# Kernel tuning notes

Hardware: AMD Instinct MI355X
Metric: run time of the kernel (lower is better)

The kernel has to match this reference:

```python
import jax, jax.numpy as jnp
import numpy as np

B, L, D, H = 2, 4096, 512, 8
HD = D // H
SCALE = 1.0 / (D / H) ** 0.5


def setup_inputs() -> dict:
    key = jax.random.key(0)
    ks = jax.random.split(key, 12)
    s = 0.02
    inp = {
        "q": jax.random.normal(ks[0], (B, L, D), jnp.float32),
        "k": jax.random.normal(ks[1], (B, L, D), jnp.float32),
        "v": jax.random.normal(ks[2], (B, L, D), jnp.float32),
        # causal mask, True = keep (masked_fill where mask == False)
        "mask": jnp.tril(jnp.ones((L, L), bool))[None, None, :, :],
        "Wq": jax.random.normal(ks[3], (D, D), jnp.float32) * s,
        "bq": jnp.zeros((D,), jnp.float32),
        "Wk": jax.random.normal(ks[4], (D, D), jnp.float32) * s,
        "bk": jnp.zeros((D,), jnp.float32),
        "Wv": jax.random.normal(ks[5], (D, D), jnp.float32) * s,
        "bv": jnp.zeros((D,), jnp.float32),
        "Wo": jax.random.normal(ks[6], (D, D), jnp.float32) * s,
        "bo": jnp.zeros((D,), jnp.float32),
    }
    return inp


def _split_heads(x):
    # [B, L, D] -> [B, H, L, HD]
    b, l, d = x.shape
    return x.reshape(b, l, H, HD).transpose(0, 2, 1, 3)


def reference(q, k, v, mask, Wq, bq, Wk, bk, Wv, bv, Wo, bo):
    # Dropout is inference-mode (identity), matching module.eval().
    qh = _split_heads(q @ Wq.T + bq)          # [B,H,L,HD]
    kh = _split_heads(k @ Wk.T + bk)          # [B,H,L,HD]
    vh = _split_heads(v @ Wv.T + bv)          # [B,H,L,HD]
    scores = jnp.einsum("bhqd,bhkd->bhqk", qh, kh) * SCALE
    scores = jnp.where(mask, scores, -jnp.inf)
    attn = jax.nn.softmax(scores, axis=-1)
    out = jnp.einsum("bhqk,bhkd->bhqd", attn, vh)  # [B,H,L,HD]
    out = out.transpose(0, 2, 1, 3).reshape(q.shape[0], q.shape[1], D)
    return out @ Wo.T + bo
```

## Files before the change

### kernel.cpp

```cpp
#include <hip/hip_runtime.h>

typedef __bf16 bf16;
typedef __bf16 bf16x4 __attribute__((ext_vector_type(4)));
typedef __bf16 bf16x8 __attribute__((ext_vector_type(8)));
typedef float  f32x4  __attribute__((ext_vector_type(4)));
typedef float  f32x16 __attribute__((ext_vector_type(16)));
typedef unsigned int u32x2 __attribute__((ext_vector_type(2)));
typedef unsigned int u32x4 __attribute__((ext_vector_type(4)));

#define NB   2
#define NL   4096
#define ND   512
#define NH   8
#define NHD  64

static __device__ __forceinline__ void g2l16(const bf16* g, bf16* l) {
    __builtin_amdgcn_global_load_lds(
        (const __attribute__((address_space(1))) unsigned int*)g,
        (__attribute__((address_space(3))) unsigned int*)l, 16, 0, 0);
}

__global__ __launch_bounds__(256, 2) void proj_qkv(
    const float* __restrict__ q, const float* __restrict__ k, const float* __restrict__ v,
    const float* __restrict__ Wq, const float* __restrict__ Wk, const float* __restrict__ Wv,
    const float* __restrict__ biasq, const float* __restrict__ biask, const float* __restrict__ biasv,
    bf16* __restrict__ qh, bf16* __restrict__ kh, bf16* __restrict__ vt)
{
    const int z = blockIdx.z;
    const float* X    = (z == 0) ? q : (z == 1) ? k : v;
    const float* W    = (z == 0) ? Wq : (z == 1) ? Wk : Wv;
    const float* bias = (z == 0) ? biasq : (z == 1) ? biask : biasv;

    const int m0 = blockIdx.y * 128;
    const int n0 = blockIdx.x * 128;

    __shared__ bf16 smem[32768];

    const int t    = threadIdx.x;
    const int lane = t & 63;
    const int wm   = (t >> 7) & 1;
    const int wn   = (t >> 6) & 1;
    const int quad = lane >> 4;
    const int l16  = lane & 15;

    f32x4 ta[8], tb[8];
    auto issue = [&](int k0) {
        #pragma unroll
        for (int p = 0; p < 8; ++p) {
            const int c4 = p * 256 + t;
            const int r = c4 >> 4, cs = c4 & 15;
            ta[p] = *(const f32x4*)(X + (size_t)(m0 + r) * ND + k0 + cs * 4);
            tb[p] = *(const f32x4*)(W + (size_t)(n0 + r) * ND + k0 + cs * 4);
        }
    };
    auto commit = [&](int buf) {
        bf16* Ad = smem + buf * 8192;
        bf16* Bd = smem + 16384 + buf * 8192;
        #pragma unroll
        for (int p = 0; p < 8; ++p) {
            const int c4 = p * 256 + t;
            const int r = c4 >> 4, cs = c4 & 15;
            const int addr = r * 64 + (((cs >> 1) ^ (r & 7)) * 8) + (cs & 1) * 4;
            bf16x4 a4, b4;
            #pragma unroll
            for (int j = 0; j < 4; ++j) { a4[j] = (bf16)ta[p][j]; b4[j] = (bf16)tb[p][j]; }
            *(bf16x4*)(Ad + addr) = a4;
            *(bf16x4*)(Bd + addr) = b4;
        }
    };

    f32x4 acc[4][4] = {};
    issue(0);

    for (int it = 0; it < 8; ++it) {
        commit(it & 1);
        __syncthreads();
        if (it + 1 < 8) issue((it + 1) * 64);

        const bf16* as = smem + (it & 1) * 8192;
        const bf16* bs = smem + 16384 + (it & 1) * 8192;
        #pragma unroll
        for (int kk = 0; kk < 2; ++kk) {
            bf16x8 aF[4], bF[4];
            #pragma unroll
            for (int i = 0; i < 4; ++i) {
                const int ra = wm * 64 + i * 16 + l16;
                const int rb = wn * 64 + i * 16 + l16;
                aF[i] = *(const bf16x8*)(as + ra * 64 + (((kk * 4 + quad) ^ (ra & 7)) * 8));
                bF[i] = *(const bf16x8*)(bs + rb * 64 + (((kk * 4 + quad) ^ (rb & 7)) * 8));
            }
            #pragma unroll
            for (int mt = 0; mt < 4; ++mt)
                #pragma unroll
                for (int nt = 0; nt < 4; ++nt)
                    acc[mt][nt] = __builtin_amdgcn_mfma_f32_16x16x32_bf16(
                        aF[mt], bF[nt], acc[mt][nt], 0, 0, 0);
        }
    }

    __syncthreads();
    const float oscale = (z == 0) ? 0.125f : (z == 1) ? 1.4426950408889634f : 1.0f;
    const int b = m0 >> 12;
    const int l0 = m0 & 4095;
    bf16* Cs = smem;

    if (z == 2) {
        #pragma unroll
        for (int nt = 0; nt < 4; ++nt) {
            const int col = wn * 64 + nt * 16 + l16;
            const float bb = bias[n0 + col];
            #pragma unroll
            for (int mt = 0; mt < 4; ++mt) {
                const int rowm = wm * 64 + mt * 16 + quad * 4;
                #pragma unroll
                for (int rb = 0; rb < 4; ++rb)
                    Cs[col * 136 + rowm + rb] = (bf16)(acc[mt][nt][rb] + bb);
            }
        }
        __syncthreads();
        #pragma unroll
        for (int p = 0; p < 8; ++p) {
            const int id = p * 256 + t;
            const int c = id >> 4, kc = id & 15;
            const int gcol = n0 + c;
            const int h = gcol >> 6, hd = gcol & 63;
            const bf16x8 v8 = *(const bf16x8*)(Cs + c * 136 + kc * 8);
            *(bf16x8*)(vt + ((size_t)(b * NH + h) * NHD + hd) * NL + l0 + kc * 8) = v8;
        }
    } else {
        #pragma unroll
        for (int nt = 0; nt < 4; ++nt) {
            const int col = wn * 64 + nt * 16 + l16;
            const float bb = bias[n0 + col];
            #pragma unroll
            for (int mt = 0; mt < 4; ++mt) {
                const int rowm = wm * 64 + mt * 16 + quad * 4;
                #pragma unroll
                for (int rb = 0; rb < 4; ++rb)
                    Cs[(rowm + rb) * 136 + col] = (bf16)((acc[mt][nt][rb] + bb) * oscale);
            }
        }
        __syncthreads();
        bf16* dst = (z == 0) ? qh : kh;
        const int h0 = n0 >> 6;
        #pragma unroll
        for (int p = 0; p < 8; ++p) {
            const int id = p * 256 + t;
            const int r = id >> 4, j = (id >> 3) & 1, kc = id & 7;
            const bf16x8 v8 = *(const bf16x8*)(Cs + r * 136 + j * 64 + kc * 8);
            *(bf16x8*)(dst + ((size_t)(b * NH + h0 + j) * NL + l0 + r) * NHD + kc * 8) = v8;
        }
    }
}

__global__ __launch_bounds__(512, 2) void attn(
    const bf16* __restrict__ qh, const bf16* __restrict__ kh,
    const bf16* __restrict__ vt, bf16* __restrict__ ao)
{
    const int bh  = blockIdx.x;
    const int b   = bh >> 3, h = bh & 7;
    const int qtA = blockIdx.y;
    const int qtB = 31 - qtA;
    const int nAp = qtA + 1;

    __shared__ bf16 smem[65536];

    const int t    = threadIdx.x;
    const int wave = t >> 6;
    const int g    = wave >> 2;
    const int w4   = wave & 3;
    const int lane = t & 63;
    const int l32  = lane & 31;
    const int half = lane >> 5;
    const int sb   = g * 32768;
    const int tg   = t & 255;

    const bf16* Qg = qh + (size_t)bh * NL * NHD;
    const bf16* Kg = kh + (size_t)bh * NL * NHD;
    const bf16* Vg = vt + (size_t)bh * NHD * NL;

    #pragma unroll
    for (int p = 0; p < 4; ++p) {
        const int id = p * 512 + t;
        const int tile = id >> 10, r = (id >> 3) & 127, s = id & 7;
        const int q0 = (tile ? qtB : qtA) * 128;
        g2l16(Qg + (size_t)(q0 + r) * NHD + s * 8, smem + id * 8);
    }
    __syncthreads();

    bf16x8 qf[4];
    {
        const int qoff = (g == 0) ? 8192 : 0;
        #pragma unroll
        for (int c = 0; c < 4; ++c)
            qf[c] = *(const bf16x8*)(smem + qoff + (w4 * 32 + l32) * 64 + c * 16 + half * 8);
    }
    __syncthreads();

    auto stage_kv = [&](int k0, int buf) {
        bf16* kd = smem + sb + buf * 16384;
        bf16* vd = kd + 8192;
        #pragma unroll
        for (int p = 0; p < 4; ++p) {
            const int id = p * 256 + tg;
            const int r = id >> 3, s = id & 7;
            g2l16(Kg + (size_t)(k0 + r) * NHD + ((s ^ (r & 7)) * 8), kd + id * 8);
            const int ks2 = id >> 9, idh = id & 511;
            const int r2 = idh >> 3, s2 = idh & 7;
            g2l16(Vg + (size_t)r2 * NL + k0 + ks2 * 64 + ((s2 ^ (r2 & 7)) * 8),
                  vd + id * 8);
        }
    };

    stage_kv(((g == 0) ? (15 - qtA) : 0) * 128, 0);

    f32x16 o_acc[2] = {};
    float l_lane = 0.f;

    for (int jj = 0; jj < 17; ++jj) {
        __syncthreads();

        if (jj + 1 < 17) {
            const int jn = jj + 1;
            if (g == 0)          stage_kv((15 - qtA + jn) * 128, jn & 1);
            else if (jn < 16)    stage_kv(((jn < nAp) ? jn : jn - nAp) * 128, jn & 1);
        }

        if (g == 1 && jj == nAp) {
            const float lt = l_lane + __shfl_xor(l_lane, 32, 64);
            const float rcp = 1.0f / fmaxf(lt, 1e-20f);
            const int row = qtA * 128 + w4 * 32 + l32;
            #pragma unroll
            for (int mt2 = 0; mt2 < 2; ++mt2)
                #pragma unroll
                for (int rr = 0; rr < 4; ++rr) {
                    const int hd = mt2 * 32 + rr * 8 + half * 4;
                    bf16x4 val;
                    #pragma unroll
                    for (int rb = 0; rb < 4; ++rb)
                        val[rb] = (bf16)(o_acc[mt2][rr * 4 + rb] * rcp);
                    *(bf16x4*)(ao + ((size_t)b * NL + row) * ND + h * NHD + hd) = val;
                }
            o_acc[0] = (f32x16)(0.f); o_acc[1] = (f32x16)(0.f);
            l_lane = 0.f;
            const bf16* Qt = Qg + (size_t)(qtB * 128 + w4 * 32 + l32) * NHD;
            #pragma unroll
            for (int c = 0; c < 4; ++c)
                qf[c] = *(const bf16x8*)(Qt + c * 16 + half * 8);
        }

        const bool act = (g == 0) || (jj < 16);
        if (act) {
            const bool onA   = (g == 1) && (jj < nAp);
            const int tile   = (g == 0) ? (15 - qtA + jj) : (onA ? jj : jj - nAp);
            const int qt_cur = onA ? qtA : qtB;
            const bf16* kb_ = smem + sb + (jj & 1) * 16384;
            const bf16* vb_ = kb_ + 8192;
            const int qrow_l = w4 * 32 + l32;

            #pragma unroll
            for (int ksub = 0; ksub < 2; ++ksub) {
                const bf16* ks_ = kb_ + ksub * 4096;
                const bf16* vs_ = vb_ + ksub * 4096;
                const int j64 = tile * 2 + ksub;

                f32x16 sacc[2] = {};
                #pragma unroll
                for (int c = 0; c < 4; ++c) {
                    #pragma unroll
                    for (int mt = 0; mt < 2; ++mt) {
                        const int row   = mt * 32 + l32;
                        const int chunk = 2 * c + half;
                        const bf16x8 kf = *(const bf16x8*)(ks_ + row * 64 + ((chunk ^ (row & 7)) * 8));
                        sacc[mt] = __builtin_amdgcn_mfma_f32_32x32x16_bf16(
                            kf, qf[c], sacc[mt], 0, 0, 0);
                    }
                }

                const bool diag = (j64 >= 2 * qt_cur);
                const int  dq   = j64 * 64 - qt_cur * 128;
                #pragma unroll
                for (int mt = 0; mt < 2; ++mt) {
                    #pragma unroll
                    for (int r = 0; r < 16; ++r) {
                        const int kv = mt * 32 + (r & 3) + 8 * (r >> 2) + 4 * half;
                        float e;
                        if (diag && (dq + kv > qrow_l)) e = 0.f;
                        else e = __builtin_amdgcn_exp2f(sacc[mt][r]);
                        l_lane += e;
                        sacc[mt][r] = e;
                    }
                }

                #pragma unroll
                for (int c = 0; c < 4; ++c) {
                    const int mt = c >> 1;
                    const int b0 = (c & 1) * 8;
                    unsigned w0, w1, w2, w3;
                    asm("v_cvt_pk_bf16_f32 %0, %1, %2" : "=v"(w0)
                        : "v"(sacc[mt][b0 + 0]), "v"(sacc[mt][b0 + 1]));
                    asm("v_cvt_pk_bf16_f32 %0, %1, %2" : "=v"(w1)
                        : "v"(sacc[mt][b0 + 2]), "v"(sacc[mt][b0 + 3]));
                    asm("v_cvt_pk_bf16_f32 %0, %1, %2" : "=v"(w2)
                        : "v"(sacc[mt][b0 + 4]), "v"(sacc[mt][b0 + 5]));
                    asm("v_cvt_pk_bf16_f32 %0, %1, %2" : "=v"(w3)
                        : "v"(sacc[mt][b0 + 6]), "v"(sacc[mt][b0 + 7]));
                    const u32x2 s02 = __builtin_amdgcn_permlane32_swap(w0, w2, false, false);
                    const u32x2 s13 = __builtin_amdgcn_permlane32_swap(w1, w3, false, false);
                    u32x4 pw_ = { s02.x, s13.x, s02.y, s13.y };
                    bf16x8 pf;
                    __builtin_memcpy(&pf, &pw_, 16);
                    #pragma unroll
                    for (int mt2 = 0; mt2 < 2; ++mt2) {
                        const int row = mt2 * 32 + l32;
                        const int u8  = 2 * c + half;
                        const bf16x8 vf = *(const bf16x8*)(vs_ + row * 64 + ((u8 ^ (row & 7)) * 8));
                        o_acc[mt2] = __builtin_amdgcn_mfma_f32_32x32x16_bf16(
                            vf, pf, o_acc[mt2], 0, 0, 0);
                    }
                }
            }
        }
    }

    __syncthreads();
    float* comb = (float*)smem;
    if (g == 1) {
        const int base = w4 * (64 * 36) + lane * 36;
        #pragma unroll
        for (int mt2 = 0; mt2 < 2; ++mt2)
            #pragma unroll
            for (int i = 0; i < 16; ++i)
                comb[base + mt2 * 16 + i] = o_acc[mt2][i];
        const float lt = l_lane + __shfl_xor(l_lane, 32, 64);
        if (half == 0) comb[9216 + w4 * 32 + l32] = lt;
    }
    __syncthreads();
    if (g == 0) {
        const int base = w4 * (64 * 36) + lane * 36;
        const float lt = l_lane + __shfl_xor(l_lane, 32, 64)
                       + comb[9216 + w4 * 32 + l32];
        const float rcp = 1.0f / fmaxf(lt, 1e-20f);
        const int row = qtB * 128 + w4 * 32 + l32;
        #pragma unroll
        for (int mt2 = 0; mt2 < 2; ++mt2)
            #pragma unroll
            for (int rr = 0; rr < 4; ++rr) {
                const int hd = mt2 * 32 + rr * 8 + half * 4;
                bf16x4 val;
                #pragma unroll
                for (int rb = 0; rb < 4; ++rb)
                    val[rb] = (bf16)((o_acc[mt2][rr * 4 + rb] +
                                      comb[base + mt2 * 16 + rr * 4 + rb]) * rcp);
                *(bf16x4*)(ao + ((size_t)b * NL + row) * ND + h * NHD + hd) = val;
            }
    }
}

__global__ __launch_bounds__(256, 2) void out_proj(
    const bf16* __restrict__ ao, const float* __restrict__ wo,
    const float* __restrict__ bo, float* __restrict__ out)
{
    const int m0 = blockIdx.y * 128;
    const int n0 = blockIdx.x * 128;

    __shared__ bf16 smem[34816];

    const int t    = threadIdx.x;
    const int lane = t & 63;
    const int wm   = (t >> 7) & 1;
    const int wn   = (t >> 6) & 1;
    const int quad = lane >> 4;
    const int l16  = lane & 15;

    bf16x8 va[4];
    f32x4  tb[8];
    auto issue = [&](int k0) {
        #pragma unroll
        for (int p = 0; p < 4; ++p) {
            const int c8 = p * 256 + t;
            const int r = c8 >> 3, s = c8 & 7;
            va[p] = *(const bf16x8*)(ao + (size_t)(m0 + r) * ND + k0 + s * 8);
        }
        #pragma unroll
        for (int p = 0; p < 8; ++p) {
            const int c4 = p * 256 + t;
            const int r = c4 >> 4, cs = c4 & 15;
            tb[p] = *(const f32x4*)(wo + (size_t)(n0 + r) * ND + k0 + cs * 4);
        }
    };
    auto commit = [&](int buf) {
        bf16* Ad = smem + buf * 8192;
        bf16* Bd = smem + 16384 + buf * 8192;
        #pragma unroll
        for (int p = 0; p < 4; ++p) {
            const int c8 = p * 256 + t;
            const int r = c8 >> 3, s = c8 & 7;
            *(bf16x8*)(Ad + r * 64 + ((s ^ (r & 7)) * 8)) = va[p];
        }
        #pragma unroll
        for (int p = 0; p < 8; ++p) {
            const int c4 = p * 256 + t;
            const int r = c4 >> 4, cs = c4 & 15;
            const int addr = r * 64 + (((cs >> 1) ^ (r & 7)) * 8) + (cs & 1) * 4;
            bf16x4 b4;
            #pragma unroll
            for (int j = 0; j < 4; ++j) b4[j] = (bf16)tb[p][j];
            *(bf16x4*)(Bd + addr) = b4;
        }
    };

    f32x4 acc[4][4] = {};
    issue(0);

    for (int it = 0; it < 8; ++it) {
        commit(it & 1);
        __syncthreads();
        if (it + 1 < 8) issue((it + 1) * 64);

        const bf16* as = smem + (it & 1) * 8192;
        const bf16* bs = smem + 16384 + (it & 1) * 8192;
        #pragma unroll
        for (int kk = 0; kk < 2; ++kk) {
            bf16x8 aF[4], bF[4];
            #pragma unroll
            for (int i = 0; i < 4; ++i) {
                const int ra = wm * 64 + i * 16 + l16;
                const int rb = wn * 64 + i * 16 + l16;
                aF[i] = *(const bf16x8*)(as + ra * 64 + (((kk * 4 + quad) ^ (ra & 7)) * 8));
                bF[i] = *(const bf16x8*)(bs + rb * 64 + (((kk * 4 + quad) ^ (rb & 7)) * 8));
            }
            #pragma unroll
            for (int mt = 0; mt < 4; ++mt)
                #pragma unroll
                for (int nt = 0; nt < 4; ++nt)
                    acc[mt][nt] = __builtin_amdgcn_mfma_f32_16x16x32_bf16(
                        aF[mt], bF[nt], acc[mt][nt], 0, 0, 0);
        }
    }

    __syncthreads();
    float* Cs = (float*)smem;
    #pragma unroll
    for (int nt = 0; nt < 4; ++nt) {
        const int col = wn * 64 + nt * 16 + l16;
        const float bb = bo[n0 + col];
        #pragma unroll
        for (int mt = 0; mt < 4; ++mt) {
            const int rowm = wm * 64 + mt * 16 + quad * 4;
            #pragma unroll
            for (int rb = 0; rb < 4; ++rb)
                Cs[(rowm + rb) * 132 + col] = acc[mt][nt][rb] + bb;
        }
    }
    __syncthreads();
    #pragma unroll
    for (int p = 0; p < 16; ++p) {
        const int id = p * 256 + t;
        const int r = id >> 5, kc = id & 31;
        const f32x4 v4 = *(const f32x4*)(Cs + r * 132 + kc * 4);
        *(f32x4*)(out + (size_t)(m0 + r) * ND + n0 + kc * 4) = v4;
    }
}

extern "C" void kernel_launch(void* const* d_in, const int* in_sizes, int n_in,
                              void* d_out, int out_size, void* d_ws, size_t ws_size,
                              hipStream_t stream) {
    (void)in_sizes; (void)n_in; (void)out_size; (void)ws_size;

    const float* q  = (const float*)d_in[0];
    const float* k  = (const float*)d_in[1];
    const float* v  = (const float*)d_in[2];
    const float* Wq = (const float*)d_in[4];
    const float* bq = (const float*)d_in[5];
    const float* Wk = (const float*)d_in[6];
    const float* bk = (const float*)d_in[7];
    const float* Wv = (const float*)d_in[8];
    const float* bv = (const float*)d_in[9];
    const float* Wo = (const float*)d_in[10];
    const float* bo = (const float*)d_in[11];

    const size_t XSZ = (size_t)NB * NL * ND;
    bf16* p = (bf16*)d_ws;
    bf16* qh  = p; p += XSZ;
    bf16* kh  = p; p += XSZ;
    bf16* vt  = p; p += XSZ;
    bf16* ao  = p; p += XSZ;

    dim3 g1(ND / 128, (NB * NL) / 128, 3);
    proj_qkv<<<g1, 256, 0, stream>>>(q, k, v, Wq, Wk, Wv, bq, bk, bv, qh, kh, vt);

    dim3 g2(16, 16, 1);
    attn<<<g2, 512, 0, stream>>>(qh, kh, vt, ao);

    dim3 g3(ND / 128, (NB * NL) / 128, 1);
    out_proj<<<g3, 256, 0, stream>>>(ao, Wo, bo, (float*)d_out);
}
```

Measured before the change: 248.7 us.

## Fuse QKV projection, attention and output projection into one persistent kernel

Result: slower. 309.3 us (+24.4%).

```diff
diff --git a/kernel.cpp b/kernel.cpp
--- a/kernel.cpp
+++ b/kernel.cpp
@@ -20,446 +20,459 @@
         (__attribute__((address_space(3))) unsigned int*)l, 16, 0, 0);
 }
 
-__global__ __launch_bounds__(256, 2) void proj_qkv(
+__device__ __forceinline__ void gbar(unsigned* c) {
+    __syncthreads();
+    if (threadIdx.x == 0) {
+        __threadfence();
+        atomicAdd(c, 1u);
+        while (atomicAdd(c, 0u) < 256u) __builtin_amdgcn_s_sleep(8);
+        __threadfence();
+    }
+    __syncthreads();
+}
+
+__global__ __launch_bounds__(512, 2) void fused(
     const float* __restrict__ q, const float* __restrict__ k, const float* __restrict__ v,
     const float* __restrict__ Wq, const float* __restrict__ Wk, const float* __restrict__ Wv,
-    const float* __restrict__ biasq, const float* __restrict__ biask, const float* __restrict__ biasv,
-    bf16* __restrict__ qh, bf16* __restrict__ kh, bf16* __restrict__ vt)
+    const float* __restrict__ bq, const float* __restrict__ bk, const float* __restrict__ bv,
+    const float* __restrict__ Wo, const float* __restrict__ bo,
+    bf16* __restrict__ qh, bf16* __restrict__ kh, bf16* __restrict__ vt,
+    bf16* __restrict__ ao, float* __restrict__ out, unsigned* __restrict__ ctr)
 {
-    const int z = blockIdx.z;
-    const float* X    = (z == 0) ? q : (z == 1) ? k : v;
-    const float* W    = (z == 0) ? Wq : (z == 1) ? Wk : Wv;
-    const float* bias = (z == 0) ? biasq : (z == 1) ? biask : biasv;
-
-    const int m0 = blockIdx.y * 128;
-    const int n0 = blockIdx.x * 128;
-
-    __shared__ bf16 smem[32768];
-
+    __shared__ bf16 smem[65536];
+
+    const int bid  = blockIdx.x;
     const int t    = threadIdx.x;
     const int lane = t & 63;
-    const int wm   = (t >> 7) & 1;
-    const int wn   = (t >> 6) & 1;
-    const int quad = lane >> 4;
-    const int l16  = lane & 15;
-
-    f32x4 ta[8], tb[8];
-    auto issue = [&](int k0) {
+
+    {
+        const int wave = t >> 6;
+        const int wm   = wave >> 2;
+        const int wn   = wave & 3;
+        const int quad = lane >> 4;
+        const int l16  = lane & 15;
+        const int m0 = (bid >> 2) * 128;
+        const int n0 = (bid & 3) * 128;
+        const int b  = m0 >> 12;
+        const int l0 = m0 & 4095;
+
+        for (int zi = 0; zi < 3; ++zi) {
+            const float* X    = (zi == 0) ? q  : (zi == 1) ? k  : v;
+            const float* W    = (zi == 0) ? Wq : (zi == 1) ? Wk : Wv;
+            const float* bias = (zi == 0) ? bq : (zi == 1) ? bk : bv;
+
+            f32x4 ta[8], tb[8];
+            auto issue = [&](int k0) {
+                #pragma unroll
+                for (int p = 0; p < 8; ++p) {
+                    const int c4 = p * 512 + t;
+                    const int r = c4 >> 5, cs = c4 & 31;
+                    ta[p] = *(const f32x4*)(X + (size_t)(m0 + r) * ND + k0 + cs * 4);
+                    tb[p] = *(const f32x4*)(W + (size_t)(n0 + r) * ND + k0 + cs * 4);
+                }
+            };
+            auto commit = [&](int buf) {
+                bf16* Ad = smem + buf * 16384;
+                bf16* Bd = smem + 32768 + buf * 16384;
+                #pragma unroll
+                for (int p = 0; p < 8; ++p) {
+                    const int c4 = p * 512 + t;
+                    const int r = c4 >> 5, cs = c4 & 31;
+                    const int addr = r * 128 + ((((cs >> 1) ^ (r & 7))) * 8) + (cs & 1) * 4;
+                    bf16x4 a4, b4;
+                    #pragma unroll
+                    for (int j = 0; j < 4; ++j) { a4[j] = (bf16)ta[p][j]; b4[j] = (bf16)tb[p][j]; }
+                    *(bf16x4*)(Ad + addr) = a4;
+                    *(bf16x4*)(Bd + addr) = b4;
+                }
+            };
+
+            f32x4 acc[4][2] = {};
+            issue(0);
+            for (int it = 0; it < 4; ++it) {
+                commit(it & 1);
+                __syncthreads();
+                if (it + 1 < 4) issue((it + 1) * 128);
+
+                const bf16* as = smem + (it & 1) * 16384;
+                const bf16* bs = smem + 32768 + (it & 1) * 16384;
+                #pragma unroll
+                for (int kk = 0; kk < 4; ++kk) {
+                    bf16x8 aF[4], bF[2];
+                    #pragma unroll
+                    for (int i = 0; i < 4; ++i) {
+                        const int ra = wm * 64 + i * 16 + l16;
+                        aF[i] = *(const bf16x8*)(as + ra * 128 + (((kk * 4 + quad) ^ (ra & 7)) * 8));
+                    }
+                    #pragma unroll
+                    for (int j = 0; j < 2; ++j) {
+                        const int rb = wn * 32 + j * 16 + l16;
+                        bF[j] = *(const bf16x8*)(bs + rb * 128 + (((kk * 4 + quad) ^ (rb & 7)) * 8));
+                    }
+                    #pragma unroll
+                    for (int mt = 0; mt < 4; ++mt)
+                        #pragma unroll
+                        for (int nt = 0; nt < 2; ++nt)
+                            acc[mt][nt] = __builtin_amdgcn_mfma_f32_16x16x32_bf16(
+                                aF[mt], bF[nt], acc[mt][nt], 0, 0, 0);
+                }
+            }
+
+            __syncthreads();
+            const float oscale = (zi == 0) ? 0.125f : (zi == 1) ? 1.4426950408889634f : 1.0f;
+            bf16* Cs = smem;
+
+            if (zi == 2) {
+                #pragma unroll
+                for (int nt = 0; nt < 2; ++nt) {
+                    const int col = wn * 32 + nt * 16 + l16;
+                    const float bb = bias[n0 + col];
+                    #pragma unroll
+                    for (int mt = 0; mt < 4; ++mt) {
+                        const int rowm = wm * 64 + mt * 16 + quad * 4;
+                        #pragma unroll
+                        for (int rb = 0; rb < 4; ++rb)
+                            Cs[col * 136 + rowm + rb] = (bf16)(acc[mt][nt][rb] + bb);
+                    }
+                }
+                __syncthreads();
+                #pragma unroll
+                for (int p = 0; p < 4; ++p) {
+                    const int id = p * 512 + t;
+                    const int c = id >> 4, kc = id & 15;
+                    const int gcol = n0 + c;
+                    const int h = gcol >> 6, hd = gcol & 63;
+                    const bf16x8 v8 = *(const bf16x8*)(Cs + c * 136 + kc * 8);
+                    *(bf16x8*)(vt + ((size_t)(b * NH + h) * NHD + hd) * NL + l0 + kc * 8) = v8;
+                }
+            } else {
+                #pragma unroll
+                for (int nt = 0; nt < 2; ++nt) {
+                    const int col = wn * 32 + nt * 16 + l16;
+                    const float bb = bias[n0 + col];
+                    #pragma unroll
+                    for (int mt = 0; mt < 4; ++mt) {
+                        const int rowm = wm * 64 + mt * 16 + quad * 4;
+                        #pragma unroll
+                        for (int rb = 0; rb < 4; ++rb)
+                            Cs[(rowm + rb) * 136 + col] = (bf16)((acc[mt][nt][rb] + bb) * oscale);
+                    }
+                }
+                __syncthreads();
+                bf16* dst = (zi == 0) ? qh : kh;
+                const int h0 = n0 >> 6;
+                #pragma unroll
+                for (int p = 0; p < 4; ++p) {
+                    const int id = p * 512 + t;
+                    const int r = id >> 4, j = (id >> 3) & 1, kc = id & 7;
+                    const bf16x8 v8 = *(const bf16x8*)(Cs + r * 136 + j * 64 + kc * 8);
+                    *(bf16x8*)(dst + ((size_t)(b * NH + h0 + j) * NL + l0 + r) * NHD + kc * 8) = v8;
+                }
+            }
+            __syncthreads();
+        }
+    }
+
+    gbar(ctr);
+
+    {
+        const int bh  = bid >> 4;
+        const int b   = bh >> 3, h = bh & 7;
+        const int qtA = bid & 15;
+        const int qtB = 31 - qtA;
+        const int nAp = qtA + 1;
+
+        const int wave = t >> 6;
+        const int g    = wave >> 2;
+        const int w4   = wave & 3;
+        const int l32  = lane & 31;
+        const int half = lane >> 5;
+        const int sb   = g * 32768;
+        const int tg   = t & 255;
+
+        const bf16* Qg = qh + (size_t)bh * NL * NHD;
+        const bf16* Kg = kh + (size_t)bh * NL * NHD;
+        const bf16* Vg = vt + (size_t)bh * NHD * NL;
+
         #pragma unroll
-        for (int p = 0; p < 8; ++p) {
-            const int c4 = p * 256 + t;
-            const int r = c4 >> 4, cs = c4 & 15;
-            ta[p] = *(const f32x4*)(X + (size_t)(m0 + r) * ND + k0 + cs * 4);
-            tb[p] = *(const f32x4*)(W + (size_t)(n0 + r) * ND + k0 + cs * 4);
-        }
-    };
-    auto commit = [&](int buf) {
-        bf16* Ad = smem + buf * 8192;
-        bf16* Bd = smem + 16384 + buf * 8192;
+        for (int p = 0; p < 4; ++p) {
+            const int id = p * 512 + t;
+            const int tile = id >> 10, r = (id >> 3) & 127, s = id & 7;
+            const int q0 = (tile ? qtB : qtA) * 128;
+            g2l16(Qg + (size_t)(q0 + r) * NHD + s * 8, smem + id * 8);
+        }
+        __syncthreads();
+
+        bf16x8 qf[4];
+        {
+            const int qoff = (g == 0) ? 8192 : 0;
+            #pragma unroll
+            for (int c = 0; c < 4; ++c)
+                qf[c] = *(const bf16x8*)(smem + qoff + (w4 * 32 + l32) * 64 + c * 16 + half * 8);
+        }
+        __syncthreads();
+
+        auto stage_kv = [&](int k0, int buf) {
+            bf16* kd = smem + sb + buf * 16384;
+            bf16* vd = kd + 8192;
+            #pragma unroll
+            for (int p = 0; p < 4; ++p) {
+                const int id = p * 256 + tg;
+                const int r = id >> 3, s = id & 7;
+                g2l16(Kg + (size_t)(k0 + r) * NHD + ((s ^ (r & 7)) * 8), kd + id * 8);
+                const int ks2 = id >> 9, idh = id & 511;
+                const int r2 = idh >> 3, s2 = idh & 7;
+                g2l16(Vg + (size_t)r2 * NL + k0 + ks2 * 64 + ((s2 ^ (r2 & 7)) * 8),
+                      vd + id * 8);
+            }
+        };
+
+        stage_kv(((g == 0) ? (15 - qtA) : 0) * 128, 0);
+
+        f32x16 o_acc[2] = {};
+        float l_lane = 0.f;
+
+        for (int jj = 0; jj < 17; ++jj) {
+            __syncthreads();
+
+            if (jj + 1 < 17) {
+                const int jn = jj + 1;
+                if (g == 0)          stage_kv((15 - qtA + jn) * 128, jn & 1);
+                else if (jn < 16)    stage_kv(((jn < nAp) ? jn : jn - nAp) * 128, jn & 1);
+            }
+
+            if (g == 1 && jj == nAp) {
+                const float lt = l_lane + __shfl_xor(l_lane, 32, 64);
+                const float rcp = 1.0f / fmaxf(lt, 1e-20f);
+                const int row = qtA * 128 + w4 * 32 + l32;
+                #pragma unroll
+                for (int mt2 = 0; mt2 < 2; ++mt2)
+                    #pragma unroll
+                    for (int rr = 0; rr < 4; ++rr) {
+                        const int hd = mt2 * 32 + rr * 8 + half * 4;
+                        bf16x4 val;
+                        #pragma unroll
+                        for (int rb = 0; rb < 4; ++rb)
+                            val[rb] = (bf16)(o_acc[mt2][rr * 4 + rb] * rcp);
+                        *(bf16x4*)(ao + ((size_t)b * NL + row) * ND + h * NHD + hd) = val;
+                    }
+                o_acc[0] = (f32x16)(0.f); o_acc[1] = (f32x16)(0.f);
+                l_lane = 0.f;
+                const bf16* Qt = Qg + (size_t)(qtB * 128 + w4 * 32 + l32) * NHD;
+                #pragma unroll
+                for (int c = 0; c < 4; ++c)
+                    qf[c] = *(const bf16x8*)(Qt + c * 16 + half * 8);
+            }
+
+            const bool act = (g == 0) || (jj < 16);
+            if (act) {
+                const bool onA   = (g == 1) && (jj < nAp);
+                const int tile   = (g == 0) ? (15 - qtA + jj) : (onA ? jj : jj - nAp);
+                const int qt_cur = onA ? qtA : qtB;
+                const bf16* kb_ = smem + sb + (jj & 1) * 16384;
+                const bf16* vb_ = kb_ + 8192;
+                const int qrow_l = w4 * 32 + l32;
+
+                #pragma unroll
+                for (int ksub = 0; ksub < 2; ++ksub) {
+                    const bf16* ks_ = kb_ + ksub * 4096;
+                    const bf16* vs_ = vb_ + ksub * 4096;
+                    const int j64 = tile * 2 + ksub;
+
+                    f32x16 sacc[2] = {};
+                    #pragma unroll
+                    for (int c = 0; c < 4; ++c) {
+                        #pragma unroll
+                        for (int mt = 0; mt < 2; ++mt) {
+                            const int row   = mt * 32 + l32;
+                            const int chunk = 2 * c + half;
+                            const bf16x8 kf = *(const bf16x8*)(ks_ + row * 64 + ((chunk ^ (row & 7)) * 8));
+                            sacc[mt] = __builtin_amdgcn_mfma_f32_32x32x16_bf16(
+                                kf, qf[c], sacc[mt], 0, 0, 0);
+                        }
+                    }
+
+                    const bool diag = (j64 >= 2 * qt_cur);
+                    const int  dq   = j64 * 64 - qt_cur * 128;
+                    #pragma unroll
+                    for (int mt = 0; mt < 2; ++mt) {
+                        #pragma unroll
+                        for (int r = 0; r < 16; ++r) {
+                            const int kv = mt * 32 + (r & 3) + 8 * (r >> 2) + 4 * half;
+                            float e;
+                            if (diag && (dq + kv > qrow_l)) e = 0.f;
+                            else e = __builtin_amdgcn_exp2f(sacc[mt][r]);
+                            l_lane += e;
+                            sacc[mt][r] = e;
+                        }
+                    }
+
+                    #pragma unroll
+                    for (int c = 0; c < 4; ++c) {
+                        const int mt = c >> 1;
+                        const int b0 = (c & 1) * 8;
+                        unsigned w0, w1, w2, w3;
+                        asm("v_cvt_pk_bf16_f32 %0, %1, %2" : "=v"(w0)
+                            : "v"(sacc[mt][b0 + 0]), "v"(sacc[mt][b0 + 1]));
+                        asm("v_cvt_pk_bf16_f32 %0, %1, %2" : "=v"(w1)
+                            : "v"(sacc[mt][b0 + 2]), "v"(sacc[mt][b0 + 3]));
+                        asm("v_cvt_pk_bf16_f32 %0, %1, %2" : "=v"(w2)
+                            : "v"(sacc[mt][b0 + 4]), "v"(sacc[mt][b0 + 5]));
+                        asm("v_cvt_pk_bf16_f32 %0, %1, %2" : "=v"(w3)
+                            : "v"(sacc[mt][b0 + 6]), "v"(sacc[mt][b0 + 7]));
+                        const u32x2 s02 = __builtin_amdgcn_permlane32_swap(w0, w2, false, false);
+                        const u32x2 s13 = __builtin_amdgcn_permlane32_swap(w1, w3, false, false);
+                        u32x4 pw_ = { s02.x, s13.x, s02.y, s13.y };
+                        bf16x8 pf;
+                        __builtin_memcpy(&pf, &pw_, 16);
+                        #pragma unroll
+                        for (int mt2 = 0; mt2 < 2; ++mt2) {
+                            const int row = mt2 * 32 + l32;
+                            const int u8  = 2 * c + half;
+                            const bf16x8 vf = *(const bf16x8*)(vs_ + row * 64 + ((u8 ^ (row & 7)) * 8));
+                            o_acc[mt2] = __builtin_amdgcn_mfma_f32_32x32x16_bf16(
+                                vf, pf, o_acc[mt2], 0, 0, 0);
+                        }
+                    }
+                }
+            }
+        }
+
+        __syncthreads();
+        float* comb = (float*)smem;
+        if (g == 1) {
+            const int base = w4 * (64 * 36) + lane * 36;
+            #pragma unroll
+            for (int mt2 = 0; mt2 < 2; ++mt2)
+                #pragma unroll
+                for (int i = 0; i < 16; ++i)
+                    comb[base + mt2 * 16 + i] = o_acc[mt2][i];
+            const float lt = l_lane + __shfl_xor(l_lane, 32, 64);
+            if (half == 0) comb[9216 + w4 * 32 + l32] = lt;
+        }
+        __syncthreads();
+        if (g == 0) {
+            const int base = w4 * (64 * 36) + lane * 36;
+            const float lt = l_lane + __shfl_xor(l_lane, 32, 64)
+                           + comb[9216 + w4 * 32 + l32];
+            const float rcp = 1.0f / fmaxf(lt, 1e-20f);
+            const int row = qtB * 128 + w4 * 32 + l32;
+            #pragma unroll
+            for (int mt2 = 0; mt2 < 2; ++mt2)
+                #pragma unroll
+                for (int rr = 0; rr < 4; ++rr) {
+                    const int hd = mt2 * 32 + rr * 8 + half * 4;
+                    bf16x4 val;
+                    #pragma unroll
+                    for (int rb = 0; rb < 4; ++rb)
+                        val[rb] = (bf16)((o_acc[mt2][rr * 4 + rb] +
+                                          comb[base + mt2 * 16 + rr * 4 + rb]) * rcp);
+                    *(bf16x4*)(ao + ((size_t)b * NL + row) * ND + h * NHD + hd) = val;
+                }
+        }
+    }
+
+    gbar(ctr + 1);
+
+    {
+        const int wave = t >> 6;
+        const int wm   = wave >> 2;
+        const int wn   = wave & 3;
+        const int quad = lane >> 4;
+        const int l16  = lane & 15;
+        const int m0 = (bid >> 2) * 128;
+        const int n0 = (bid & 3) * 128;
+
+        bf16x8 va[4];
+        f32x4  tb[8];
+        auto issue = [&](int k0) {
+            #pragma unroll
+            for (int p = 0; p < 4; ++p) {
+                const int c8 = p * 512 + t;
+                const int r = c8 >> 4, s = c8 & 15;
+                va[p] = *(const bf16x8*)(ao + (size_t)(m0 + r) * ND + k0 + s * 8);
+            }
+            #pragma unroll
+            for (int p = 0; p < 8; ++p) {
+                const int c4 = p * 512 + t;
+                const int r = c4 >> 5, cs = c4 & 31;
+                tb[p] = *(const f32x4*)(Wo + (size_t)(n0 + r) * ND + k0 + cs * 4);
+            }
+        };
+        auto commit = [&](int buf) {
+            bf16* Ad = smem + buf * 16384;
+            bf16* Bd = smem + 32768 + buf * 16384;
+            #pragma unroll
+            for (int p = 0; p < 4; ++p) {
+                const int c8 = p * 512 + t;
+                const int r = c8 >> 4, s = c8 & 15;
+                *(bf16x8*)(Ad + r * 128 + ((s ^ (r & 7)) * 8)) = va[p];
+            }
+            #pragma unroll
+            for (int p = 0; p < 8; ++p) {
+                const int c4 = p * 512 + t;
+                const int r = c4 >> 5, cs = c4 & 31;
+                const int addr = r * 128 + ((((cs >> 1) ^ (r & 7))) * 8) + (cs & 1) * 4;
+                bf16x4 b4;
+                #pragma unroll
+                for (int j = 0; j < 4; ++j) b4[j] = (bf16)tb[p][j];
+                *(bf16x4*)(Bd + addr) = b4;
+            }
+        };
+
+        f32x4 acc[4][2] = {};
+        issue(0);
+        for (int it = 0; it < 4; ++it) {
+            commit(it & 1);
+            __syncthreads();
+            if (it + 1 < 4) issue((it + 1) * 128);
+
+            const bf16* as = smem + (it & 1) * 16384;
+            const bf16* bs = smem + 32768 + (it & 1) * 16384;
+            #pragma unroll
+            for (int kk = 0; kk < 4; ++kk) {
+                bf16x8 aF[4], bF[2];
+                #pragma unroll
+                for (int i = 0; i < 4; ++i) {
+                    const int ra = wm * 64 + i * 16 + l16;
+                    aF[i] = *(const bf16x8*)(as + ra * 128 + (((kk * 4 + quad) ^ (ra & 7)) * 8));
+                }
+                #pragma unroll
+                for (int j = 0; j < 2; ++j) {
+                    const int rb = wn * 32 + j * 16 + l16;
+                    bF[j] = *(const bf16x8*)(bs + rb * 128 + (((kk * 4 + quad) ^ (rb & 7)) * 8));
+                }
+                #pragma unroll
+                for (int mt = 0; mt < 4; ++mt)
+                    #pragma unroll
+                    for (int nt = 0; nt < 2; ++nt)
+                        acc[mt][nt] = __builtin_amdgcn_mfma_f32_16x16x32_bf16(
+                            aF[mt], bF[nt], acc[mt][nt], 0, 0, 0);
+            }
+        }
+
+        __syncthreads();
+        float* Cs = (float*)smem;
         #pragma unroll
-        for (int p = 0; p < 8; ++p) {
-            const int c4 = p * 256 + t;
-            const int r = c4 >> 4, cs = c4 & 15;
-            const int addr = r * 64 + (((cs >> 1) ^ (r & 7)) * 8) + (cs & 1) * 4;
-            bf16x4 a4, b4;
-            #pragma unroll
-            for (int j = 0; j < 4; ++j) { a4[j] = (bf16)ta[p][j]; b4[j] = (bf16)tb[p][j]; }
-            *(bf16x4*)(Ad + addr) = a4;
-            *(bf16x4*)(Bd + addr) = b4;
-        }
-    };
-
-    f32x4 acc[4][4] = {};
-    issue(0);
-
-    for (int it = 0; it < 8; ++it) {
-        commit(it & 1);
-        __syncthreads();
-        if (it + 1 < 8) issue((it + 1) * 64);
-
-        const bf16* as = smem + (it & 1) * 8192;
-        const bf16* bs = smem + 16384 + (it & 1) * 8192;
-        #pragma unroll
-        for (int kk = 0; kk < 2; ++kk) {
-            bf16x8 aF[4], bF[4];
-            #pragma unroll
-            for (int i = 0; i < 4; ++i) {
-                const int ra = wm * 64 + i * 16 + l16;
-                const int rb = wn * 64 + i * 16 + l16;
-                aF[i] = *(const bf16x8*)(as + ra * 64 + (((kk * 4 + quad) ^ (ra & 7)) * 8));
-                bF[i] = *(const bf16x8*)(bs + rb * 64 + (((kk * 4 + quad) ^ (rb & 7)) * 8));
-            }
-            #pragma unroll
-            for (int mt = 0; mt < 4; ++mt)
-                #pragma unroll
-                for (int nt = 0; nt < 4; ++nt)
-                    acc[mt][nt] = __builtin_amdgcn_mfma_f32_16x16x32_bf16(
-                        aF[mt], bF[nt], acc[mt][nt], 0, 0, 0);
-        }
-    }
-
-    __syncthreads();
-    const float oscale = (z == 0) ? 0.125f : (z == 1) ? 1.4426950408889634f : 1.0f;
-    const int b = m0 >> 12;
-    const int l0 = m0 & 4095;
-    bf16* Cs = smem;
-
-    if (z == 2) {
-        #pragma unroll
-        for (int nt = 0; nt < 4; ++nt) {
-            const int col = wn * 64 + nt * 16 + l16;
-            const float bb = bias[n0 + col];
+        for (int nt = 0; nt < 2; ++nt) {
+            const int col = wn * 32 + nt * 16 + l16;
+            const float bb = bo[n0 + col];
             #pragma unroll
             for (int mt = 0; mt < 4; ++mt) {
                 const int rowm = wm * 64 + mt * 16 + quad * 4;
                 #pragma unroll
                 for (int rb = 0; rb < 4; ++rb)
-                    Cs[col * 136 + rowm + rb] = (bf16)(acc[mt][nt][rb] + bb);
+                    Cs[(rowm + rb) * 132 + col] = acc[mt][nt][rb] + bb;
             }
         }
         __syncthreads();
         #pragma unroll
         for (int p = 0; p < 8; ++p) {
-            const int id = p * 256 + t;
-            const int c = id >> 4, kc = id & 15;
-            const int gcol = n0 + c;
-            const int h = gcol >> 6, hd = gcol & 63;
-            const bf16x8 v8 = *(const bf16x8*)(Cs + c * 136 + kc * 8);
-            *(bf16x8*)(vt + ((size_t)(b * NH + h) * NHD + hd) * NL + l0 + kc * 8) = v8;
-        }
-    } else {
-        #pragma unroll
-        for (int nt = 0; nt < 4; ++nt) {
-            const int col = wn * 64 + nt * 16 + l16;
-            const float bb = bias[n0 + col];
-            #pragma unroll
-            for (int mt = 0; mt < 4; ++mt) {
-                const int rowm = wm * 64 + mt * 16 + quad * 4;
-                #pragma unroll
-                for (int rb = 0; rb < 4; ++rb)
-                    Cs[(rowm + rb) * 136 + col] = (bf16)((acc[mt][nt][rb] + bb) * oscale);
-            }
-        }
-        __syncthreads();
-        bf16* dst = (z == 0) ? qh : kh;
-        const int h0 = n0 >> 6;
-        #pragma unroll
-        for (int p = 0; p < 8; ++p) {
-            const int id = p * 256 + t;
-            const int r = id >> 4, j = (id >> 3) & 1, kc = id & 7;
-            const bf16x8 v8 = *(const bf16x8*)(Cs + r * 136 + j * 64 + kc * 8);
-            *(bf16x8*)(dst + ((size_t)(b * NH + h0 + j) * NL + l0 + r) * NHD + kc * 8) = v8;
-        }
-    }
-}
-
-__global__ __launch_bounds__(512, 2) void attn(
-    const bf16* __restrict__ qh, const bf16* __restrict__ kh,
-    const bf16* __restrict__ vt, bf16* __restrict__ ao)
-{
-    const int bh  = blockIdx.x;
-    const int b   = bh >> 3, h = bh & 7;
-    const int qtA = blockIdx.y;
-    const int qtB = 31 - qtA;
-    const int nAp = qtA + 1;
-
-    __shared__ bf16 smem[65536];
-
-    const int t    = threadIdx.x;
-    const int wave = t >> 6;
-    const int g    = wave >> 2;
-    const int w4   = wave & 3;
-    const int lane = t & 63;
-    const int l32  = lane & 31;
-    const int half = lane >> 5;
-    const int sb   = g * 32768;
-    const int tg   = t & 255;
-
-    const bf16* Qg = qh + (size_t)bh * NL * NHD;
-    const bf16* Kg = kh + (size_t)bh * NL * NHD;
-    const bf16* Vg = vt + (size_t)bh * NHD * NL;
-
-    #pragma unroll
-    for (int p = 0; p < 4; ++p) {
-        const int id = p * 512 + t;
-        const int tile = id >> 10, r = (id >> 3) & 127, s = id & 7;
-        const int q0 = (tile ? qtB : qtA) * 128;
-        g2l16(Qg + (size_t)(q0 + r) * NHD + s * 8, smem + id * 8);
-    }
-    __syncthreads();
-
-    bf16x8 qf[4];
-    {
-        const int qoff = (g == 0) ? 8192 : 0;
-        #pragma unroll
-        for (int c = 0; c < 4; ++c)
-            qf[c] = *(const bf16x8*)(smem + qoff + (w4 * 32 + l32) * 64 + c * 16 + half * 8);
-    }
-    __syncthreads();
-
-    auto stage_kv = [&](int k0, int buf) {
-        bf16* kd = smem + sb + buf * 16384;
-        bf16* vd = kd + 8192;
-        #pragma unroll
-        for (int p = 0; p < 4; ++p) {
-            const int id = p * 256 + tg;
-            const int r = id >> 3, s = id & 7;
-            g2l16(Kg + (size_t)(k0 + r) * NHD + ((s ^ (r & 7)) * 8), kd + id * 8);
-            const int ks2 = id >> 9, idh = id & 511;
-            const int r2 = idh >> 3, s2 = idh & 7;
-            g2l16(Vg + (size_t)r2 * NL + k0 + ks2 * 64 + ((s2 ^ (r2 & 7)) * 8),
-                  vd + id * 8);
-        }
-    };
-
-    stage_kv(((g == 0) ? (15 - qtA) : 0) * 128, 0);
-
-    f32x16 o_acc[2] = {};
-    float l_lane = 0.f;
-
-    for (int jj = 0; jj < 17; ++jj) {
-        __syncthreads();
-
-        if (jj + 1 < 17) {
-            const int jn = jj + 1;
-            if (g == 0)          stage_kv((15 - qtA + jn) * 128, jn & 1);
-            else if (jn < 16)    stage_kv(((jn < nAp) ? jn : jn - nAp) * 128, jn & 1);
-        }
-
-        if (g == 1 && jj == nAp) {
-            const float lt = l_lane + __shfl_xor(l_lane, 32, 64);
-            const float rcp = 1.0f / fmaxf(lt, 1e-20f);
-            const int row = qtA * 128 + w4 * 32 + l32;
-            #pragma unroll
-            for (int mt2 = 0; mt2 < 2; ++mt2)
-                #pragma unroll
-                for (int rr = 0; rr < 4; ++rr) {
-                    const int hd = mt2 * 32 + rr * 8 + half * 4;
-                    bf16x4 val;
-                    #pragma unroll
-                    for (int rb = 0; rb < 4; ++rb)
-                        val[rb] = (bf16)(o_acc[mt2][rr * 4 + rb] * rcp);
-                    *(bf16x4*)(ao + ((size_t)b * NL + row) * ND + h * NHD + hd) = val;
-                }
-            o_acc[0] = (f32x16)(0.f); o_acc[1] = (f32x16)(0.f);
-            l_lane = 0.f;
-            const bf16* Qt = Qg + (size_t)(qtB * 128 + w4 * 32 + l32) * NHD;
-            #pragma unroll
-            for (int c = 0; c < 4; ++c)
-                qf[c] = *(const bf16x8*)(Qt + c * 16 + half * 8);
-        }
-
-        const bool act = (g == 0) || (jj < 16);
-        if (act) {
-            const bool onA   = (g == 1) && (jj < nAp);
-            const int tile   = (g == 0) ? (15 - qtA + jj) : (onA ? jj : jj - nAp);
-            const int qt_cur = onA ? qtA : qtB;
-            const bf16* kb_ = smem + sb + (jj & 1) * 16384;
-            const bf16* vb_ = kb_ + 8192;
-            const int qrow_l = w4 * 32 + l32;
-
-            #pragma unroll
-            for (int ksub = 0; ksub < 2; ++ksub) {
-                const bf16* ks_ = kb_ + ksub * 4096;
-                const bf16* vs_ = vb_ + ksub * 4096;
-                const int j64 = tile * 2 + ksub;
-
-                f32x16 sacc[2] = {};
-                #pragma unroll
-                for (int c = 0; c < 4; ++c) {
-                    #pragma unroll
-                    for (int mt = 0; mt < 2; ++mt) {
-                        const int row   = mt * 32 + l32;
-                        const int chunk = 2 * c + half;
-                        const bf16x8 kf = *(const bf16x8*)(ks_ + row * 64 + ((chunk ^ (row & 7)) * 8));
-                        sacc[mt] = __builtin_amdgcn_mfma_f32_32x32x16_bf16(
-                            kf, qf[c], sacc[mt], 0, 0, 0);
-                    }
-                }
-
-                const bool diag = (j64 >= 2 * qt_cur);
-                const int  dq   = j64 * 64 - qt_cur * 128;
-                #pragma unroll
-                for (int mt = 0; mt < 2; ++mt) {
-                    #pragma unroll
-                    for (int r = 0; r < 16; ++r) {
-                        const int kv = mt * 32 + (r & 3) + 8 * (r >> 2) + 4 * half;
-                        float e;
-                        if (diag && (dq + kv > qrow_l)) e = 0.f;
-                        else e = __builtin_amdgcn_exp2f(sacc[mt][r]);
-                        l_lane += e;
-                        sacc[mt][r] = e;
-                    }
-                }
-
-                #pragma unroll
-                for (int c = 0; c < 4; ++c) {
-                    const int mt = c >> 1;
-                    const int b0 = (c & 1) * 8;
-                    unsigned w0, w1, w2, w3;
-                    asm("v_cvt_pk_bf16_f32 %0, %1, %2" : "=v"(w0)
-                        : "v"(sacc[mt][b0 + 0]), "v"(sacc[mt][b0 + 1]));
-                    asm("v_cvt_pk_bf16_f32 %0, %1, %2" : "=v"(w1)
-                        : "v"(sacc[mt][b0 + 2]), "v"(sacc[mt][b0 + 3]));
-                    asm("v_cvt_pk_bf16_f32 %0, %1, %2" : "=v"(w2)
-                        : "v"(sacc[mt][b0 + 4]), "v"(sacc[mt][b0 + 5]));
-                    asm("v_cvt_pk_bf16_f32 %0, %1, %2" : "=v"(w3)
-                        : "v"(sacc[mt][b0 + 6]), "v"(sacc[mt][b0 + 7]));
-                    const u32x2 s02 = __builtin_amdgcn_permlane32_swap(w0, w2, false, false);
-                    const u32x2 s13 = __builtin_amdgcn_permlane32_swap(w1, w3, false, false);
-                    u32x4 pw_ = { s02.x, s13.x, s02.y, s13.y };
-                    bf16x8 pf;
-                    __builtin_memcpy(&pf, &pw_, 16);
-                    #pragma unroll
-                    for (int mt2 = 0; mt2 < 2; ++mt2) {
-                        const int row = mt2 * 32 + l32;
-                        const int u8  = 2 * c + half;
-                        const bf16x8 vf = *(const bf16x8*)(vs_ + row * 64 + ((u8 ^ (row & 7)) * 8));
-                        o_acc[mt2] = __builtin_amdgcn_mfma_f32_32x32x16_bf16(
-                            vf, pf, o_acc[mt2], 0, 0, 0);
-                    }
-                }
-            }
-        }
-    }
-
-    __syncthreads();
-    float* comb = (float*)smem;
-    if (g == 1) {
-        const int base = w4 * (64 * 36) + lane * 36;
-        #pragma unroll
-        for (int mt2 = 0; mt2 < 2; ++mt2)
-            #pragma unroll
-            for (int i = 0; i < 16; ++i)
-                comb[base + mt2 * 16 + i] = o_acc[mt2][i];
-        const float lt = l_lane + __shfl_xor(l_lane, 32, 64);
-        if (half == 0) comb[9216 + w4 * 32 + l32] = lt;
-    }
-    __syncthreads();
-    if (g == 0) {
-        const int base = w4 * (64 * 36) + lane * 36;
-        const float lt = l_lane + __shfl_xor(l_lane, 32, 64)
-                       + comb[9216 + w4 * 32 + l32];
-        const float rcp = 1.0f / fmaxf(lt, 1e-20f);
-        const int row = qtB * 128 + w4 * 32 + l32;
-        #pragma unroll
-        for (int mt2 = 0; mt2 < 2; ++mt2)
-            #pragma unroll
-            for (int rr = 0; rr < 4; ++rr) {
-                const int hd = mt2 * 32 + rr * 8 + half * 4;
-                bf16x4 val;
-                #pragma unroll
-                for (int rb = 0; rb < 4; ++rb)
-                    val[rb] = (bf16)((o_acc[mt2][rr * 4 + rb] +
-                                      comb[base + mt2 * 16 + rr * 4 + rb]) * rcp);
-                *(bf16x4*)(ao + ((size_t)b * NL + row) * ND + h * NHD + hd) = val;
-            }
-    }
-}
-
-__global__ __launch_bounds__(256, 2) void out_proj(
-    const bf16* __restrict__ ao, const float* __restrict__ wo,
-    const float* __restrict__ bo, float* __restrict__ out)
-{
-    const int m0 = blockIdx.y * 128;
-    const int n0 = blockIdx.x * 128;
-
-    __shared__ bf16 smem[34816];
-
-    const int t    = threadIdx.x;
-    const int lane = t & 63;
-    const int wm   = (t >> 7) & 1;
-    const int wn   = (t >> 6) & 1;
-    const int quad = lane >> 4;
-    const int l16  = lane & 15;
-
-    bf16x8 va[4];
-    f32x4  tb[8];
-    auto issue = [&](int k0) {
-        #pragma unroll
-        for (int p = 0; p < 4; ++p) {
-            const int c8 = p * 256 + t;
-            const int r = c8 >> 3, s = c8 & 7;
-            va[p] = *(const bf16x8*)(ao + (size_t)(m0 + r) * ND + k0 + s * 8);
-        }
-        #pragma unroll
-        for (int p = 0; p < 8; ++p) {
-            const int c4 = p * 256 + t;
-            const int r = c4 >> 4, cs = c4 & 15;
-            tb[p] = *(const f32x4*)(wo + (size_t)(n0 + r) * ND + k0 + cs * 4);
-        }
-    };
-    auto commit = [&](int buf) {
-        bf16* Ad = smem + buf * 8192;
-        bf16* Bd = smem + 16384 + buf * 8192;
-        #pragma unroll
-        for (int p = 0; p < 4; ++p) {
-            const int c8 = p * 256 + t;
-            const int r = c8 >> 3, s = c8 & 7;
-            *(bf16x8*)(Ad + r * 64 + ((s ^ (r & 7)) * 8)) = va[p];
-        }
-        #pragma unroll
-        for (int p = 0; p < 8; ++p) {
-            const int c4 = p * 256 + t;
-            const int r = c4 >> 4, cs = c4 & 15;
-            const int addr = r * 64 + (((cs >> 1) ^ (r & 7)) * 8) + (cs & 1) * 4;
-            bf16x4 b4;
-            #pragma unroll
-            for (int j = 0; j < 4; ++j) b4[j] = (bf16)tb[p][j];
-            *(bf16x4*)(Bd + addr) = b4;
-        }
-    };
-
-    f32x4 acc[4][4] = {};
-    issue(0);
-
-    for (int it = 0; it < 8; ++it) {
-        commit(it & 1);
-        __syncthreads();
-        if (it + 1 < 8) issue((it + 1) * 64);
-
-        const bf16* as = smem + (it & 1) * 8192;
-        const bf16* bs = smem + 16384 + (it & 1) * 8192;
-        #pragma unroll
-        for (int kk = 0; kk < 2; ++kk) {
-            bf16x8 aF[4], bF[4];
-            #pragma unroll
-            for (int i = 0; i < 4; ++i) {
-                const int ra = wm * 64 + i * 16 + l16;
-                const int rb = wn * 64 + i * 16 + l16;
-                aF[i] = *(const bf16x8*)(as + ra * 64 + (((kk * 4 + quad) ^ (ra & 7)) * 8));
-                bF[i] = *(const bf16x8*)(bs + rb * 64 + (((kk * 4 + quad) ^ (rb & 7)) * 8));
-            }
-            #pragma unroll
-            for (int mt = 0; mt < 4; ++mt)
-                #pragma unroll
-                for (int nt = 0; nt < 4; ++nt)
-                    acc[mt][nt] = __builtin_amdgcn_mfma_f32_16x16x32_bf16(
-                        aF[mt], bF[nt], acc[mt][nt], 0, 0, 0);
-        }
-    }
-
-    __syncthreads();
-    float* Cs = (float*)smem;
-    #pragma unroll
-    for (int nt = 0; nt < 4; ++nt) {
-        const int col = wn * 64 + nt * 16 + l16;
-        const float bb = bo[n0 + col];
-        #pragma unroll
-        for (int mt = 0; mt < 4; ++mt) {
-            const int rowm = wm * 64 + mt * 16 + quad * 4;
-            #pragma unroll
-            for (int rb = 0; rb < 4; ++rb)
-                Cs[(rowm + rb) * 132 + col] = acc[mt][nt][rb] + bb;
-        }
-    }
-    __syncthreads();
-    #pragma unroll
-    for (int p = 0; p < 16; ++p) {
-        const int id = p * 256 + t;
-        const int r = id >> 5, kc = id & 31;
-        const f32x4 v4 = *(const f32x4*)(Cs + r * 132 + kc * 4);
-        *(f32x4*)(out + (size_t)(m0 + r) * ND + n0 + kc * 4) = v4;
+            const int id = p * 512 + t;
+            const int r = id >> 5, kc = id & 31;
+            const f32x4 v4 = *(const f32x4*)(Cs + r * 132 + kc * 4);
+            *(f32x4*)(out + (size_t)(m0 + r) * ND + n0 + kc * 4) = v4;
+        }
     }
 }
 
@@ -486,13 +499,11 @@
     bf16* kh  = p; p += XSZ;
     bf16* vt  = p; p += XSZ;
     bf16* ao  = p; p += XSZ;
-
-    dim3 g1(ND / 128, (NB * NL) / 128, 3);
-    proj_qkv<<<g1, 256, 0, stream>>>(q, k, v, Wq, Wk, Wv, bq, bk, bv, qh, kh, vt);
-
-    dim3 g2(16, 16, 1);
-    attn<<<g2, 512, 0, stream>>>(qh, kh, vt, ao);
-
-    dim3 g3(ND / 128, (NB * NL) / 128, 1);
-    out_proj<<<g3, 256, 0, stream>>>(ao, Wo, bo, (float*)d_out);
+    unsigned* ctr = (unsigned*)p;
+
+    hipMemsetAsync(ctr, 0, 8, stream);
+
+    fused<<<dim3(256), dim3(512), 0, stream>>>(
+        q, k, v, Wq, Wk, Wv, bq, bk, bv, Wo, bo,
+        qh, kh, vt, ao, (float*)d_out, ctr);
 }
```
